# Optimization experiments

Hardware: AMD Instinct MI355X
Metric: run time of the kernel (lower is better)

Reference implementation:

```python
import jax, jax.numpy as jnp
import numpy as np

HC = 4
C = 2048
TMAX = 8
RMS_EPS = 1e-6
PRE_EPS = 1e-4
SINK_EPS = 1e-6
POST_MULT = 2.0


def setup_inputs() -> dict:
    key = jax.random.key(0)
    k1, k2, k3 = jax.random.split(key, 3)
    B, S = 2, 2048
    x = jax.random.normal(k1, (B, S, HC, C), dtype=jnp.float32)
    phi = jax.random.normal(k2, (HC * C, HC * HC + 2 * HC), dtype=jnp.float32) * 0.02
    b = jnp.zeros((HC * HC + 2 * HC,), dtype=jnp.float32)
    alpha_pre = jnp.ones((), dtype=jnp.float32)
    alpha_post = jnp.ones((), dtype=jnp.float32)
    alpha_res = jnp.ones((), dtype=jnp.float32)
    W = jax.random.normal(k3, (C, C), dtype=jnp.float32) * 0.02
    Wb = jnp.zeros((C,), dtype=jnp.float32)
    return {"x": x, "phi": phi, "b": b, "alpha_pre": alpha_pre,
            "alpha_post": alpha_post, "alpha_res": alpha_res, "W": W, "Wb": Wb}


def _coeffs(x, phi, b, alpha_pre, alpha_post, alpha_res):
    # x: [..., hc, c] -> flatten streams, RMSNorm over k = hc*c
    lead = x.shape[:-2]
    flat = x.reshape(lead + (HC * C,))
    xn = flat * jax.lax.rsqrt(jnp.mean(flat * flat, axis=-1, keepdims=True) + RMS_EPS)
    logits = xn @ phi + b  # [..., hc*hc + 2*hc]
    pre = logits[..., :HC]
    post = logits[..., HC:2 * HC]
    res = logits[..., 2 * HC:].reshape(lead + (HC, HC))
    h_pre = jax.nn.sigmoid(alpha_pre * pre) + PRE_EPS          # [..., hc]
    h_post = POST_MULT * jax.nn.sigmoid(alpha_post * post)     # [..., hc]
    # Sinkhorn normalization -> approximately doubly-stochastic hc x hc matrix
    M = jnp.exp(alpha_res * res)

    def step(m, _):
        m = m / (jnp.sum(m, axis=-1, keepdims=True) + SINK_EPS)
        m = m / (jnp.sum(m, axis=-2, keepdims=True) + SINK_EPS)
        return m, None

    h_res, _ = jax.lax.scan(step, M, None, length=TMAX)
    return h_pre, h_post, h_res


def reference(x, phi, b, alpha_pre, alpha_post, alpha_res, W, Wb):
    xf = x.astype(jnp.float32)
    h_pre, h_post, h_res = _coeffs(xf, phi, b, alpha_pre, alpha_post, alpha_res)
    # combine streams into single layer input: [..., c]
    x_in = jnp.sum(xf * h_pre[..., None], axis=-2)
    f_out = x_in @ W + Wb  # the wrapped layer (Linear)
    # residual stream mixing + broadcasted post-scaled layer output
    x_out = jnp.einsum('...oi,...ic->...oc', h_res, xf) + h_post[..., None] * f_out[..., None, :]
    return x_out.astype(x.dtype)
```

## Files before the change

kernel.cpp:

```cpp
#include <hip/hip_runtime.h>
#include <hip/hip_bf16.h>

#define HCn 4
#define Cn 2048
#define Dn (HCn*Cn)
#define NLg 24
#define TMAXn 8

typedef short bf16x8 __attribute__((ext_vector_type(8)));
typedef float f32x4 __attribute__((ext_vector_type(4)));

__device__ __forceinline__ unsigned int pk2(float a, float b) {
  union { __hip_bfloat162 h; unsigned int u; } v;
  v.h = __float22bfloat162_rn(float2{a, b});
  return v.u;
}
__device__ __forceinline__ float sigm(float z) { return 1.0f / (1.0f + expf(-z)); }

__device__ __forceinline__ void gload_lds16(const void* g, void* l) {
  __builtin_amdgcn_global_load_lds((__attribute__((address_space(1))) void*)(g),
                                   (__attribute__((address_space(3))) void*)(l),
                                   16, 0, 0);
}

__global__ __launch_bounds__(128) void phib_kernel(const float* __restrict__ phi,
                                                   unsigned short* __restrict__ phiB) {
  int tid = threadIdx.x;
  int nt = tid >> 6, lane = tid & 63;
  int ks = blockIdx.x;
  int col = nt * 16 + (lane & 15);
  int kb = ks * 32 + (lane >> 4) * 8;
  float v[8];
#pragma unroll
  for (int e = 0; e < 8; ++e)
    v[e] = (col < NLg) ? phi[(size_t)(kb + e) * NLg + col] : 0.f;
  uint4 o = { pk2(v[0], v[1]), pk2(v[2], v[3]), pk2(v[4], v[5]), pk2(v[6], v[7]) };
  *(uint4*)&phiB[((size_t)(ks * 2 + nt) * 64 + lane) * 8] = o;
}

__global__ __launch_bounds__(512) void coeffs_kernel(
    const float* __restrict__ x, const unsigned short* __restrict__ phiB,
    const float* __restrict__ bb, const float* __restrict__ apre_p,
    const float* __restrict__ apost_p, const float* __restrict__ ares_p,
    unsigned int* __restrict__ xin, float* __restrict__ hpost, float* __restrict__ hres) {
  __shared__ float lgp[8][16][33];
  __shared__ float ssp[8][16];
  __shared__ float hpre_s[16][HCn];

  int tid = threadIdx.x, lane = tid & 63, wid = tid >> 6;
  long t0 = (long)blockIdx.x * 16;
  const float* xblk = x + (size_t)t0 * Dn;

  int l15 = lane & 15, kg = lane >> 4;
  const float* xr = xblk + (size_t)l15 * Dn + wid * 1024 + kg * 8;
  const bf16x8* pB = (const bf16x8*)phiB + (size_t)wid * 32 * 128 + lane;

  float ss = 0.f;
  f32x4 acc0 = {0.f,0.f,0.f,0.f}, acc1 = {0.f,0.f,0.f,0.f};

#define LOADIT(IT, P0, P1, B0, B1) {            \
    P0 = *(const float4*)(xr + (IT) * 32);      \
    P1 = *(const float4*)(xr + (IT) * 32 + 4);  \
    B0 = pB[(IT) * 128];                        \
    B1 = pB[(IT) * 128 + 64]; }

#define PROCIT(P0, P1, B0, B1) {                                              \
    ss += P0.x*P0.x + P0.y*P0.y + P0.z*P0.z + P0.w*P0.w;                      \
    ss += P1.x*P1.x + P1.y*P1.y + P1.z*P1.z + P1.w*P1.w;                      \
    uint4 u_ = { pk2(P0.x,P0.y), pk2(P0.z,P0.w), pk2(P1.x,P1.y), pk2(P1.z,P1.w) }; \
    bf16x8 a_ = *(bf16x8*)&u_;                                                \
    acc0 = __builtin_amdgcn_mfma_f32_16x16x32_bf16(a_, B0, acc0, 0, 0, 0);    \
    acc1 = __builtin_amdgcn_mfma_f32_16x16x32_bf16(a_, B1, acc1, 0, 0, 0); }

  {
    float4 pA0, pA1, qA0, qA1; bf16x8 bA0, bA1, bB0, bB1;
    LOADIT(0, pA0, pA1, bA0, bA1);
#pragma unroll
    for (int it = 0; it < 32; it += 2) {
      LOADIT(it + 1, qA0, qA1, bB0, bB1);
      PROCIT(pA0, pA1, bA0, bA1);
      if (it + 2 < 32) LOADIT(it + 2, pA0, pA1, bA0, bA1);
      PROCIT(qA0, qA1, bB0, bB1);
    }
  }
#undef LOADIT
#undef PROCIT

  ss += __shfl_xor(ss, 16); ss += __shfl_xor(ss, 32);
  if (kg == 0) ssp[wid][l15] = ss;
#pragma unroll
  for (int e = 0; e < 4; ++e) {
    int tok = kg * 4 + e;
    lgp[wid][tok][l15] = acc0[e];
    lgp[wid][tok][16 + l15] = acc1[e];
  }
  __syncthreads();

  if (tid < 16) {
    long t = t0 + tid;
    float st = 0.f;
#pragma unroll
    for (int w = 0; w < 8; ++w) st += ssp[w][tid];
    float r = rsqrtf(st / (float)Dn + 1e-6f);
    float apre = apre_p[0], apost = apost_p[0], ares = ares_p[0];
    float lg[NLg];
#pragma unroll
    for (int j = 0; j < NLg; ++j) {
      float d = 0.f;
#pragma unroll
      for (int w = 0; w < 8; ++w) d += lgp[w][tid][j];
      lg[j] = r * d + bb[j];
    }
#pragma unroll
    for (int j = 0; j < 4; ++j) hpre_s[tid][j] = sigm(apre * lg[j]) + 1e-4f;
#pragma unroll
    for (int j = 0; j < 4; ++j) hpost[t * 4 + j] = 2.0f * sigm(apost * lg[4 + j]);
    float m[16];
#pragma unroll
    for (int q = 0; q < 16; ++q) m[q] = expf(ares * lg[8 + q]);
    for (int it = 0; it < TMAXn; ++it) {
#pragma unroll
      for (int o = 0; o < 4; ++o) {
        float rs = m[o*4] + m[o*4+1] + m[o*4+2] + m[o*4+3] + 1e-6f;
        m[o*4] /= rs; m[o*4+1] /= rs; m[o*4+2] /= rs; m[o*4+3] /= rs;
      }
#pragma unroll
      for (int i = 0; i < 4; ++i) {
        float cs = m[i] + m[4+i] + m[8+i] + m[12+i] + 1e-6f;
        m[i] /= cs; m[4+i] /= cs; m[8+i] /= cs; m[12+i] /= cs;
      }
    }
#pragma unroll
    for (int q = 0; q < 16; ++q) hres[t * 16 + q] = m[q];
  }
  __syncthreads();

  int t = tid >> 5, l32 = tid & 31;
  const float4* xt = (const float4*)(xblk + (size_t)t * Dn);
  float h0 = hpre_s[t][0], h1 = hpre_s[t][1], h2 = hpre_s[t][2], h3 = hpre_s[t][3];
  uint2* xo = (uint2*)xin + (size_t)(t0 + t) * (Cn / 4);
#pragma unroll
  for (int itc = 0; itc < 16; ++itc) {
    int c4 = itc * 32 + l32;
    float4 v0 = xt[c4];
    float4 v1 = xt[c4 + 512];
    float4 v2 = xt[c4 + 1024];
    float4 v3 = xt[c4 + 1536];
    float sx = h0*v0.x + h1*v1.x + h2*v2.x + h3*v3.x;
    float sy = h0*v0.y + h1*v1.y + h2*v2.y + h3*v3.y;
    float sz = h0*v0.z + h1*v1.z + h2*v2.z + h3*v3.z;
    float sw = h0*v0.w + h1*v1.w + h2*v2.w + h3*v3.w;
    uint2 o; o.x = pk2(sx, sy); o.y = pk2(sz, sw);
    xo[c4] = o;
  }
}

__global__ __launch_bounds__(256) void wtrans_kernel(const float* __restrict__ W,
                                                     unsigned short* __restrict__ Wt) {
  __shared__ float tile[64][65];
  int kb = blockIdx.y * 64, nb = blockIdx.x * 64;
  int tr = threadIdx.x >> 4;
  int tc = threadIdx.x & 15;
#pragma unroll
  for (int rr = 0; rr < 64; rr += 16) {
    float4 v = *(const float4*)&W[(size_t)(kb + tr + rr) * Cn + nb + tc * 4];
    tile[tr + rr][tc * 4 + 0] = v.x; tile[tr + rr][tc * 4 + 1] = v.y;
    tile[tr + rr][tc * 4 + 2] = v.z; tile[tr + rr][tc * 4 + 3] = v.w;
  }
  __syncthreads();
#pragma unroll
  for (int rr = 0; rr < 64; rr += 16) {
    int n = nb + tr + rr;
    uint2 o;
    o.x = pk2(tile[tc * 4 + 0][tr + rr], tile[tc * 4 + 1][tr + rr]);
    o.y = pk2(tile[tc * 4 + 2][tr + rr], tile[tc * 4 + 3][tr + rr]);
    *(uint2*)&Wt[(size_t)n * Cn + kb + tc * 4] = o;
  }
}

#define BMt 128
#define BNt 128
#define BKt 32
#define GK Cn
__global__ __launch_bounds__(256) void gemm_ep_kernel(
    const unsigned short* __restrict__ xin, const unsigned short* __restrict__ Wt,
    const float* __restrict__ x, const float* __restrict__ Wb,
    const float* __restrict__ hpost, const float* __restrict__ hres,
    float* __restrict__ out) {
  __shared__ __align__(16) unsigned short As[BMt * BKt];
  __shared__ __align__(16) unsigned short Bs[BNt * BKt];
  int tid = threadIdx.x;
  int lane = tid & 63, wid = tid >> 6;
  int wr = wid >> 1, wc = wid & 1;
  int l15 = lane & 15, l4 = lane >> 4;
  int wg = blockIdx.x;
  wg = (wg & 7) * 64 + (wg >> 3);
  int bx = wg & 15, by = wg >> 4;

  f32x4 acc[4][4];
#pragma unroll
  for (int i = 0; i < 4; ++i)
#pragma unroll
    for (int j = 0; j < 4; ++j) acc[i][j] = {0.f, 0.f, 0.f, 0.f};

  const char* Ab = (const char*)xin + (size_t)by * BMt * GK * 2;
  const char* Bb = (const char*)Wt + (size_t)bx * BNt * GK * 2;
  int off0 = tid * 16, off1 = tid * 16 + 4096;
  int row0 = off0 >> 6, colb0 = off0 & 63;
  int row1 = off1 >> 6, colb1 = off1 & 63;

  for (int k0 = 0; k0 < GK; k0 += BKt) {
    gload_lds16(Ab + (size_t)row0 * (GK * 2) + k0 * 2 + colb0, (char*)As + off0);
    gload_lds16(Ab + (size_t)row1 * (GK * 2) + k0 * 2 + colb1, (char*)As + off1);
    gload_lds16(Bb + (size_t)row0 * (GK * 2) + k0 * 2 + colb0, (char*)Bs + off0);
    gload_lds16(Bb + (size_t)row1 * (GK * 2) + k0 * 2 + colb1, (char*)Bs + off1);
    __syncthreads();
    bf16x8 af[4], bfv[4];
#pragma unroll
    for (int fm = 0; fm < 4; ++fm)
      af[fm] = *(const bf16x8*)&As[(wr * 64 + fm * 16 + l15) * BKt + l4 * 8];
#pragma unroll
    for (int fn = 0; fn < 4; ++fn)
      bfv[fn] = *(const bf16x8*)&Bs[(wc * 64 + fn * 16 + l15) * BKt + l4 * 8];
#pragma unroll
    for (int fm = 0; fm < 4; ++fm)
#pragma unroll
      for (int fn = 0; fn < 4; ++fn)
        acc[fm][fn] = __builtin_amdgcn_mfma_f32_16x16x32_bf16(af[fm], bfv[fn], acc[fm][fn], 0, 0, 0);
    __syncthreads();
  }

  int m0 = by * BMt + wr * 64;
  int n0 = bx * BNt + wc * 64;
#pragma unroll
  for (int fm = 0; fm < 4; ++fm) {
#pragma unroll
    for (int e = 0; e < 4; ++e) {
      int t = m0 + fm * 16 + l4 * 4 + e;
      const float* hr = hres + (size_t)t * 16;
      const float* hq = hpost + (size_t)t * 4;
      const float* xt = x + (size_t)t * Dn;
      float* ot = out + (size_t)t * Dn;
      float hr_[16], hq_[4];
#pragma unroll
      for (int q = 0; q < 16; ++q) hr_[q] = hr[q];
#pragma unroll
      for (int q = 0; q < 4; ++q) hq_[q] = hq[q];
#pragma unroll
      for (int fn = 0; fn < 4; ++fn) {
        int c = n0 + fn * 16 + l15;
        float f = acc[fm][fn][e] + Wb[c];
        float x0 = xt[c], x1 = xt[Cn + c], x2 = xt[2 * Cn + c], x3 = xt[3 * Cn + c];
#pragma unroll
        for (int o = 0; o < 4; ++o) {
          ot[(size_t)o * Cn + c] =
              hq_[o] * f + hr_[o*4+0] * x0 + hr_[o*4+1] * x1 + hr_[o*4+2] * x2 + hr_[o*4+3] * x3;
        }
      }
    }
  }
}

extern "C" void kernel_launch(void* const* d_in, const int* in_sizes, int n_in,
                              void* d_out, int out_size, void* d_ws, size_t ws_size,
                              hipStream_t stream) {
  const float* x     = (const float*)d_in[0];
  const float* phi   = (const float*)d_in[1];
  const float* b     = (const float*)d_in[2];
  const float* apre  = (const float*)d_in[3];
  const float* apost = (const float*)d_in[4];
  const float* ares  = (const float*)d_in[5];
  const float* W     = (const float*)d_in[6];
  const float* Wb    = (const float*)d_in[7];
  float* out = (float*)d_out;

  int NT = in_sizes[0] / Dn;
  char* ws = (char*)d_ws;
  size_t xin_b = (size_t)NT * Cn * 2;
  size_t wt_b  = (size_t)Cn * Cn * 2;
  size_t hp_b  = (size_t)NT * 4 * 4;
  size_t hr_b  = (size_t)NT * 16 * 4;
  unsigned int*   xin  = (unsigned int*)ws;
  unsigned short* Wt   = (unsigned short*)(ws + xin_b);
  float* hpost = (float*)(ws + xin_b + wt_b);
  float* hres  = (float*)(ws + xin_b + wt_b + hp_b);
  unsigned short* phiB = (unsigned short*)(ws + xin_b + wt_b + hp_b + hr_b);

  hipLaunchKernelGGL(phib_kernel, dim3(Dn / 32), dim3(128), 0, stream, phi, phiB);
  hipLaunchKernelGGL(coeffs_kernel, dim3(NT / 16), dim3(512), 0, stream,
                     x, phiB, b, apre, apost, ares, xin, hpost, hres);
  hipLaunchKernelGGL(wtrans_kernel, dim3(Cn / 64, Cn / 64), dim3(256), 0, stream, W, Wt);
  hipLaunchKernelGGL(gemm_ep_kernel, dim3((Cn / BNt) * (NT / BMt)), dim3(256), 0, stream,
                     (const unsigned short*)xin, Wt, x, Wb, hpost, hres, out);
}
```

Before: 177.8 us.

## Split coeffs kernel into split-K logits, finalize, and xin kernels

Splits the fused coefficient kernel into three stages. The logits kernel splits the K dimension four ways, giving four times as many blocks, and writes partial logits and sum-of-squares to a buffer. A small finalize kernel reduces the partials and computes the sigmoids and the Sinkhorn normalization. A separate xin kernel builds the bf16 combined input. The aim is better GPU occupancy with only 256 tokens-per-16 blocks, at the cost of re-reading x from memory in a separate pass plus extra launches.

```diff
diff --git a/kernel.cpp b/kernel.cpp
--- a/kernel.cpp
+++ b/kernel.cpp
@@ -38,50 +38,45 @@
   *(uint4*)&phiB[((size_t)(ks * 2 + nt) * 64 + lane) * 8] = o;
 }
 
-__global__ __launch_bounds__(512) void coeffs_kernel(
+__global__ __launch_bounds__(512) void logits_kernel(
     const float* __restrict__ x, const unsigned short* __restrict__ phiB,
-    const float* __restrict__ bb, const float* __restrict__ apre_p,
-    const float* __restrict__ apost_p, const float* __restrict__ ares_p,
-    unsigned int* __restrict__ xin, float* __restrict__ hpost, float* __restrict__ hres) {
+    float* __restrict__ pbuf) {
   __shared__ float lgp[8][16][33];
   __shared__ float ssp[8][16];
-  __shared__ float hpre_s[16][HCn];
 
   int tid = threadIdx.x, lane = tid & 63, wid = tid >> 6;
-  long t0 = (long)blockIdx.x * 16;
-  const float* xblk = x + (size_t)t0 * Dn;
-
+  int g = blockIdx.x >> 2;
+  int kc = blockIdx.x & 3;
+  long t0 = (long)g * 16;
   int l15 = lane & 15, kg = lane >> 4;
-  const float* xr = xblk + (size_t)l15 * Dn + wid * 1024 + kg * 8;
-  const bf16x8* pB = (const bf16x8*)phiB + (size_t)wid * 32 * 128 + lane;
+
+  int kbase = kc * 2048 + wid * 256;
+  const float* xr = x + (size_t)(t0 + l15) * Dn + kbase + kg * 8;
+  const bf16x8* pB = (const bf16x8*)phiB + (size_t)(kbase >> 5) * 128 + lane;
 
   float ss = 0.f;
   f32x4 acc0 = {0.f,0.f,0.f,0.f}, acc1 = {0.f,0.f,0.f,0.f};
 
-#define LOADIT(IT, P0, P1, B0, B1) {            \
-    P0 = *(const float4*)(xr + (IT) * 32);      \
-    P1 = *(const float4*)(xr + (IT) * 32 + 4);  \
-    B0 = pB[(IT) * 128];                        \
-    B1 = pB[(IT) * 128 + 64]; }
-
-#define PROCIT(P0, P1, B0, B1) {                                              \
+  float4 A0[3], A1[3]; bf16x8 Bv0[3], Bv1[3];
+#define LOADIT(IT, S) {                          \
+    A0[S] = *(const float4*)(xr + (IT) * 32);    \
+    A1[S] = *(const float4*)(xr + (IT) * 32 + 4);\
+    Bv0[S] = pB[(IT) * 128];                     \
+    Bv1[S] = pB[(IT) * 128 + 64]; }
+#define PROCIT(S) {                                                           \
+    float4 P0 = A0[S], P1 = A1[S];                                            \
     ss += P0.x*P0.x + P0.y*P0.y + P0.z*P0.z + P0.w*P0.w;                      \
     ss += P1.x*P1.x + P1.y*P1.y + P1.z*P1.z + P1.w*P1.w;                      \
     uint4 u_ = { pk2(P0.x,P0.y), pk2(P0.z,P0.w), pk2(P1.x,P1.y), pk2(P1.z,P1.w) }; \
     bf16x8 a_ = *(bf16x8*)&u_;                                                \
-    acc0 = __builtin_amdgcn_mfma_f32_16x16x32_bf16(a_, B0, acc0, 0, 0, 0);    \
-    acc1 = __builtin_amdgcn_mfma_f32_16x16x32_bf16(a_, B1, acc1, 0, 0, 0); }
-
-  {
-    float4 pA0, pA1, qA0, qA1; bf16x8 bA0, bA1, bB0, bB1;
-    LOADIT(0, pA0, pA1, bA0, bA1);
-#pragma unroll
-    for (int it = 0; it < 32; it += 2) {
-      LOADIT(it + 1, qA0, qA1, bB0, bB1);
-      PROCIT(pA0, pA1, bA0, bA1);
-      if (it + 2 < 32) LOADIT(it + 2, pA0, pA1, bA0, bA1);
-      PROCIT(qA0, qA1, bB0, bB1);
-    }
+    acc0 = __builtin_amdgcn_mfma_f32_16x16x32_bf16(a_, Bv0[S], acc0, 0, 0, 0);\
+    acc1 = __builtin_amdgcn_mfma_f32_16x16x32_bf16(a_, Bv1[S], acc1, 0, 0, 0); }
+
+  LOADIT(0, 0); LOADIT(1, 1);
+#pragma unroll
+  for (int it = 0; it < 8; ++it) {
+    if (it < 6) LOADIT(it + 2, (it + 2) % 3);
+    PROCIT(it % 3);
   }
 #undef LOADIT
 #undef PROCIT
@@ -96,52 +91,70 @@
   }
   __syncthreads();
 
-  if (tid < 16) {
-    long t = t0 + tid;
-    float st = 0.f;
-#pragma unroll
-    for (int w = 0; w < 8; ++w) st += ssp[w][tid];
-    float r = rsqrtf(st / (float)Dn + 1e-6f);
-    float apre = apre_p[0], apost = apost_p[0], ares = ares_p[0];
-    float lg[NLg];
-#pragma unroll
-    for (int j = 0; j < NLg; ++j) {
-      float d = 0.f;
-#pragma unroll
-      for (int w = 0; w < 8; ++w) d += lgp[w][tid][j];
-      lg[j] = r * d + bb[j];
+  for (int q = tid; q < 16 * 25; q += 512) {
+    int tk = q / 25, j = q % 25;
+    float v = 0.f;
+    if (j < 24) {
+#pragma unroll
+      for (int w = 0; w < 8; ++w) v += lgp[w][tk][j];
+    } else {
+#pragma unroll
+      for (int w = 0; w < 8; ++w) v += ssp[w][tk];
     }
-#pragma unroll
-    for (int j = 0; j < 4; ++j) hpre_s[tid][j] = sigm(apre * lg[j]) + 1e-4f;
-#pragma unroll
-    for (int j = 0; j < 4; ++j) hpost[t * 4 + j] = 2.0f * sigm(apost * lg[4 + j]);
-    float m[16];
-#pragma unroll
-    for (int q = 0; q < 16; ++q) m[q] = expf(ares * lg[8 + q]);
-    for (int it = 0; it < TMAXn; ++it) {
-#pragma unroll
-      for (int o = 0; o < 4; ++o) {
-        float rs = m[o*4] + m[o*4+1] + m[o*4+2] + m[o*4+3] + 1e-6f;
-        m[o*4] /= rs; m[o*4+1] /= rs; m[o*4+2] /= rs; m[o*4+3] /= rs;
-      }
-#pragma unroll
-      for (int i = 0; i < 4; ++i) {
-        float cs = m[i] + m[4+i] + m[8+i] + m[12+i] + 1e-6f;
-        m[i] /= cs; m[4+i] /= cs; m[8+i] /= cs; m[12+i] /= cs;
-      }
+    pbuf[(size_t)(t0 + tk) * 100 + kc * 25 + j] = v;
+  }
+}
+
+__global__ __launch_bounds__(256) void finalize_kernel(
+    const float* __restrict__ pbuf, const float* __restrict__ bb,
+    const float* __restrict__ apre_p, const float* __restrict__ apost_p,
+    const float* __restrict__ ares_p, float* __restrict__ hpre,
+    float* __restrict__ hpost, float* __restrict__ hres) {
+  long t = (long)blockIdx.x * 256 + threadIdx.x;
+  const float* pt = pbuf + (size_t)t * 100;
+  float lg[25];
+#pragma unroll
+  for (int j = 0; j < 25; ++j)
+    lg[j] = pt[j] + pt[25 + j] + pt[50 + j] + pt[75 + j];
+  float r = rsqrtf(lg[24] / (float)Dn + 1e-6f);
+  float apre = apre_p[0], apost = apost_p[0], ares = ares_p[0];
+#pragma unroll
+  for (int j = 0; j < NLg; ++j) lg[j] = r * lg[j] + bb[j];
+#pragma unroll
+  for (int j = 0; j < 4; ++j) hpre[t * 4 + j] = sigm(apre * lg[j]) + 1e-4f;
+#pragma unroll
+  for (int j = 0; j < 4; ++j) hpost[t * 4 + j] = 2.0f * sigm(apost * lg[4 + j]);
+  float m[16];
+#pragma unroll
+  for (int q = 0; q < 16; ++q) m[q] = expf(ares * lg[8 + q]);
+  for (int it = 0; it < TMAXn; ++it) {
+#pragma unroll
+    for (int o = 0; o < 4; ++o) {
+      float rs = m[o*4] + m[o*4+1] + m[o*4+2] + m[o*4+3] + 1e-6f;
+      m[o*4] /= rs; m[o*4+1] /= rs; m[o*4+2] /= rs; m[o*4+3] /= rs;
     }
 #pragma unroll
-    for (int q = 0; q < 16; ++q) hres[t * 16 + q] = m[q];
-  }
-  __syncthreads();
-
-  int t = tid >> 5, l32 = tid & 31;
-  const float4* xt = (const float4*)(xblk + (size_t)t * Dn);
-  float h0 = hpre_s[t][0], h1 = hpre_s[t][1], h2 = hpre_s[t][2], h3 = hpre_s[t][3];
-  uint2* xo = (uint2*)xin + (size_t)(t0 + t) * (Cn / 4);
-#pragma unroll
-  for (int itc = 0; itc < 16; ++itc) {
-    int c4 = itc * 32 + l32;
+    for (int i = 0; i < 4; ++i) {
+      float cs = m[i] + m[4+i] + m[8+i] + m[12+i] + 1e-6f;
+      m[i] /= cs; m[4+i] /= cs; m[8+i] /= cs; m[12+i] /= cs;
+    }
+  }
+#pragma unroll
+  for (int q = 0; q < 16; ++q) hres[t * 16 + q] = m[q];
+}
+
+__global__ __launch_bounds__(256) void xin_kernel(
+    const float* __restrict__ x, const float* __restrict__ hpre,
+    unsigned int* __restrict__ xin) {
+  long t = blockIdx.x;
+  int tid = threadIdx.x;
+  float h0 = hpre[t * 4 + 0], h1 = hpre[t * 4 + 1];
+  float h2 = hpre[t * 4 + 2], h3 = hpre[t * 4 + 3];
+  const float4* xt = (const float4*)(x + (size_t)t * Dn);
+  uint2* xo = (uint2*)xin + (size_t)t * (Cn / 4);
+#pragma unroll
+  for (int it = 0; it < 2; ++it) {
+    int c4 = it * 256 + tid;
     float4 v0 = xt[c4];
     float4 v1 = xt[c4 + 512];
     float4 v2 = xt[c4 + 1024];
@@ -276,19 +289,21 @@
 
   int NT = in_sizes[0] / Dn;
   char* ws = (char*)d_ws;
-  size_t xin_b = (size_t)NT * Cn * 2;
-  size_t wt_b  = (size_t)Cn * Cn * 2;
-  size_t hp_b  = (size_t)NT * 4 * 4;
-  size_t hr_b  = (size_t)NT * 16 * 4;
-  unsigned int*   xin  = (unsigned int*)ws;
-  unsigned short* Wt   = (unsigned short*)(ws + xin_b);
-  float* hpost = (float*)(ws + xin_b + wt_b);
-  float* hres  = (float*)(ws + xin_b + wt_b + hp_b);
-  unsigned short* phiB = (unsigned short*)(ws + xin_b + wt_b + hp_b + hr_b);
+  size_t off = 0;
+  unsigned int*   xin  = (unsigned int*)(ws + off);   off += (size_t)NT * Cn * 2;
+  unsigned short* Wt   = (unsigned short*)(ws + off); off += (size_t)Cn * Cn * 2;
+  float* hpre  = (float*)(ws + off); off += (size_t)NT * 4 * 4;
+  float* hpost = (float*)(ws + off); off += (size_t)NT * 4 * 4;
+  float* hres  = (float*)(ws + off); off += (size_t)NT * 16 * 4;
+  unsigned short* phiB = (unsigned short*)(ws + off); off += (size_t)Dn * 32 * 2;
+  float* pbuf  = (float*)(ws + off); off += (size_t)NT * 100 * 4;
 
   hipLaunchKernelGGL(phib_kernel, dim3(Dn / 32), dim3(128), 0, stream, phi, phiB);
-  hipLaunchKernelGGL(coeffs_kernel, dim3(NT / 16), dim3(512), 0, stream,
-                     x, phiB, b, apre, apost, ares, xin, hpost, hres);
+  hipLaunchKernelGGL(logits_kernel, dim3((NT / 16) * 4), dim3(512), 0, stream,
+                     x, phiB, pbuf);
+  hipLaunchKernelGGL(finalize_kernel, dim3(NT / 256), dim3(256), 0, stream,
+                     pbuf, b, apre, apost, ares, hpre, hpost, hres);
+  hipLaunchKernelGGL(xin_kernel, dim3(NT), dim3(256), 0, stream, x, hpre, xin);
   hipLaunchKernelGGL(wtrans_kernel, dim3(Cn / 64, Cn / 64), dim3(256), 0, stream, W, Wt);
   hipLaunchKernelGGL(gemm_ep_kernel, dim3((Cn / BNt) * (NT / BMt)), dim3(256), 0, stream,
                      (const unsigned short*)xin, Wt, x, Wb, hpost, hres, out);
```

Result: faster. 164.3 us (-7.6%).
